# Kernel optimization log

Measured on AMD Instinct MI355X. Metric: run time of the kernel, lower is better.

The kernel has to match this reference:

```python
import math
import jax, jax.numpy as jnp
import numpy as np

B, S, M, D, H, FF = 2, 2048, 64, 1024, 16, 4096
HD = D // H


def setup_inputs() -> dict:
    key = jax.random.key(0)
    ks = jax.random.split(key, 16)
    w = lambda k, shape: jax.random.normal(k, shape, dtype=jnp.float32) * 0.02
    # RoPE angles: theta_i = pos / 10000^(2i/head_dim)
    inv_freq = 1.0 / (10000.0 ** (jnp.arange(0, HD, 2, dtype=jnp.float32) / HD))
    ang = jnp.arange(S, dtype=jnp.float32)[:, None] * inv_freq[None, :]  # (S, HD//2)
    return {
        "tgt": jax.random.normal(ks[0], (B, S, D), dtype=jnp.float32),
        "memory": jax.random.normal(ks[1], (B, M, D), dtype=jnp.float32),
        "rope_cos": jnp.cos(ang),
        "rope_sin": jnp.sin(ang),
        "W_qkv": w(ks[2], (D, 3 * D)), "b_qkv": jnp.zeros((3 * D,), jnp.float32),
        "W_o": w(ks[3], (D, D)), "b_o": jnp.zeros((D,), jnp.float32),
        "Wq_c": w(ks[4], (D, D)), "bq_c": jnp.zeros((D,), jnp.float32),
        "Wk_c": w(ks[5], (D, D)), "bk_c": jnp.zeros((D,), jnp.float32),
        "Wv_c": w(ks[6], (D, D)), "bv_c": jnp.zeros((D,), jnp.float32),
        "W_co": w(ks[7], (D, D)), "b_co": jnp.zeros((D,), jnp.float32),
        "W1": w(ks[8], (D, FF)), "b1": jnp.zeros((FF,), jnp.float32),
        "W2": w(ks[9], (FF, D)), "b2": jnp.zeros((D,), jnp.float32),
        "g1": jnp.ones((D,), jnp.float32), "be1": jnp.zeros((D,), jnp.float32),
        "g2": jnp.ones((D,), jnp.float32), "be2": jnp.zeros((D,), jnp.float32),
        "g3": jnp.ones((D,), jnp.float32), "be3": jnp.zeros((D,), jnp.float32),
    }


def _layer_norm(x, g, b, eps=1e-5):
    mu = jnp.mean(x, axis=-1, keepdims=True)
    var = jnp.mean(jnp.square(x - mu), axis=-1, keepdims=True)
    return (x - mu) * jax.lax.rsqrt(var + eps) * g + b


def _apply_rope(x, cos, sin):
    # x: (B, H, S, HD); cos/sin: (S, HD//2). Pairs (even, odd) rotated as complex.
    xe, xo = x[..., 0::2], x[..., 1::2]
    c = cos[None, None]
    s = sin[None, None]
    re = xe * c - xo * s
    im = xe * s + xo * c
    return jnp.stack([re, im], axis=-1).reshape(x.shape)


def reference(tgt, memory, rope_cos, rope_sin, W_qkv, b_qkv, W_o, b_o,
              Wq_c, bq_c, Wk_c, bk_c, Wv_c, bv_c, W_co, b_co,
              W1, b1, W2, b2, g1, be1, g2, be2, g3, be3):
    b, s, d = tgt.shape
    scale = 1.0 / math.sqrt(HD)

    # --- RoPE self-attention (causal) ---
    x = _layer_norm(tgt, g1, be1)
    qkv = (x @ W_qkv + b_qkv).reshape(b, s, 3, H, HD)
    qkv = jnp.transpose(qkv, (2, 0, 3, 1, 4))  # (3, b, H, s, HD)
    q, k, v = qkv[0], qkv[1], qkv[2]
    q = _apply_rope(q, rope_cos[:s], rope_sin[:s])
    k = _apply_rope(k, rope_cos[:s], rope_sin[:s])
    attn = jnp.einsum('bhqd,bhkd->bhqk', q, k) * scale
    causal = jnp.tril(jnp.ones((s, s), dtype=bool))
    attn = jnp.where(causal[None, None], attn, -1e9)
    attn = jax.nn.softmax(attn, axis=-1)
    sa = jnp.einsum('bhqk,bhkd->bhqd', attn, v)
    sa = jnp.transpose(sa, (0, 2, 1, 3)).reshape(b, s, d)
    tgt = tgt + (sa @ W_o + b_o)

    # --- cross-attention to memory (no positional encoding) ---
    x = _layer_norm(tgt, g2, be2)
    m = memory.shape[1]
    qc = (x @ Wq_c + bq_c).reshape(b, s, H, HD).transpose(0, 2, 1, 3)
    kc = (memory @ Wk_c + bk_c).reshape(b, m, H, HD).transpose(0, 2, 1, 3)
    vc = (memory @ Wv_c + bv_c).reshape(b, m, H, HD).transpose(0, 2, 1, 3)
    ca = jax.nn.softmax(jnp.einsum('bhqd,bhkd->bhqk', qc, kc) * scale, axis=-1)
    co = jnp.einsum('bhqk,bhkd->bhqd', ca, vc)
    co = jnp.transpose(co, (0, 2, 1, 3)).reshape(b, s, d)
    tgt = tgt + (co @ W_co + b_co)

    # --- FFN (exact GELU, dropout disabled = eval) ---
    x = _layer_norm(tgt, g3, be3)
    ffn = jax.nn.gelu(x @ W1 + b1, approximate=False) @ W2 + b2
    return tgt + ffn
```

## Files before the change

### kernel.cpp

```cpp
#include <hip/hip_runtime.h>

typedef unsigned short u16;
typedef short bf16x8 __attribute__((ext_vector_type(8)));
typedef float f32x4 __attribute__((ext_vector_type(4)));

#define HN 16
#define SD 64
#define SEQ 2048
#define DM 1024
#define QSC 0.18033688f

__device__ __forceinline__ float bf2f(u16 h) {
  return __uint_as_float(((unsigned int)h) << 16);
}
__device__ __forceinline__ u16 f2bf(float f) {
  unsigned int x = __float_as_uint(f);
  x += 0x7fffu + ((x >> 16) & 1u);
  return (u16)(x >> 16);
}
__device__ __forceinline__ float geluf(float x) {
  return 0.5f * x * (1.0f + erff(x * 0.70710678118654752f));
}
__device__ __forceinline__ void load_lds16(const u16* g, u16* l) {
  __builtin_amdgcn_global_load_lds(
      (const __attribute__((address_space(1))) void*)g,
      (__attribute__((address_space(3))) void*)l, 16, 0, 0);
}

__device__ __forceinline__ void trans_tile(const float* __restrict__ in,
                                           u16* __restrict__ out, int K, int N,
                                           int tx, int ty, int tid,
                                           u16 (*T)[72]) {
  const int n0 = tx * 64, k0 = ty * 64;
#pragma unroll
  for (int it = 0; it < 2; ++it) {
    const int t = it * 256 + tid, r = t >> 3, c = (t & 7) * 8;
    const float* src = &in[(size_t)(k0 + r) * N + n0 + c];
    float4 d0 = *(const float4*)src;
    float4 d1 = *(const float4*)(src + 4);
    T[r][c + 0] = f2bf(d0.x);
    T[r][c + 1] = f2bf(d0.y);
    T[r][c + 2] = f2bf(d0.z);
    T[r][c + 3] = f2bf(d0.w);
    T[r][c + 4] = f2bf(d1.x);
    T[r][c + 5] = f2bf(d1.y);
    T[r][c + 6] = f2bf(d1.z);
    T[r][c + 7] = f2bf(d1.w);
  }
  __syncthreads();
#pragma unroll
  for (int it = 0; it < 2; ++it) {
    const int t = it * 256 + tid, r = t >> 3, c = (t & 7) * 8;
    uint4 d;
    u16* p = (u16*)&d;
#pragma unroll
    for (int j = 0; j < 8; ++j) p[j] = T[c + j][r];
    *(uint4*)&out[(size_t)(n0 + r) * K + k0 + c] = d;
  }
}

__global__ __launch_bounds__(256) void prep1(
    const float* __restrict__ Wqkv, const float* __restrict__ Wo,
    const float* __restrict__ Wqc, const float* __restrict__ Wkc,
    const float* __restrict__ Wvc, const float* __restrict__ Wco,
    u16* __restrict__ Tqkv, u16* __restrict__ To, u16* __restrict__ Tqc,
    u16* __restrict__ Tkc, u16* __restrict__ Tvc, u16* __restrict__ Tco,
    const float* __restrict__ mem, u16* __restrict__ memb) {
  __shared__ u16 T[64][72];
  const int t = blockIdx.x, tid = threadIdx.x;
  if (t < 768) {
    trans_tile(Wqkv, Tqkv, 1024, 3072, t % 48, t / 48, tid, T);
    return;
  }
  if (t < 2048) {
    const int u = t - 768, m = u >> 8, sub = u & 255;
    const float* in;
    u16* out;
    if (m == 0) { in = Wo; out = To; }
    else if (m == 1) { in = Wqc; out = Tqc; }
    else if (m == 2) { in = Wkc; out = Tkc; }
    else if (m == 3) { in = Wvc; out = Tvc; }
    else { in = Wco; out = Tco; }
    trans_tile(in, out, 1024, 1024, sub & 15, sub >> 4, tid, T);
    return;
  }
  const int i = ((t - 2048) * 256 + tid) * 4;
  float4 d = *(const float4*)&mem[i];
  uint2 o;
  u16* po = (u16*)&o;
  po[0] = f2bf(d.x);
  po[1] = f2bf(d.y);
  po[2] = f2bf(d.z);
  po[3] = f2bf(d.w);
  *(uint2*)&memb[i] = o;
}

__global__ __launch_bounds__(256) void prep2(const float* __restrict__ W1,
                                             const float* __restrict__ W2,
                                             u16* __restrict__ T1,
                                             u16* __restrict__ T2) {
  __shared__ u16 T[64][72];
  const int t = blockIdx.x, tid = threadIdx.x;
  if (t < 1024) {
    trans_tile(W1, T1, 1024, 4096, t & 63, t >> 6, tid, T);
  } else {
    const int u = t - 1024;
    trans_tile(W2, T2, 4096, 1024, u & 15, u >> 4, tid, T);
  }
}

__global__ __launch_bounds__(256) void ln_kernel(
    const float* __restrict__ x, const float* __restrict__ g,
    const float* __restrict__ be, u16* __restrict__ y) {
  const int row = blockIdx.x, tid = threadIdx.x;
  const float* xr = x + (size_t)row * DM;
  float4 d = *(const float4*)&xr[tid * 4];
  float v[4] = {d.x, d.y, d.z, d.w};
  float s1 = 0.f, s2 = 0.f;
#pragma unroll
  for (int j = 0; j < 4; ++j) {
    s1 += v[j];
    s2 += v[j] * v[j];
  }
#pragma unroll
  for (int dd = 1; dd < 64; dd <<= 1) {
    s1 += __shfl_xor(s1, dd, 64);
    s2 += __shfl_xor(s2, dd, 64);
  }
  __shared__ float p1[4], p2[4];
  const int lane = tid & 63, wv = tid >> 6;
  if (lane == 0) {
    p1[wv] = s1;
    p2[wv] = s2;
  }
  __syncthreads();
  s1 = p1[0] + p1[1] + p1[2] + p1[3];
  s2 = p2[0] + p2[1] + p2[2] + p2[3];
  const float mu = s1 * (1.f / DM);
  const float rs = rsqrtf(fmaxf(s2 * (1.f / DM) - mu * mu, 0.f) + 1e-5f);
  float4 gg = *(const float4*)&g[tid * 4];
  float4 bb = *(const float4*)&be[tid * 4];
  const float gv[4] = {gg.x, gg.y, gg.z, gg.w};
  const float bv[4] = {bb.x, bb.y, bb.z, bb.w};
  uint2 o;
  u16* po = (u16*)&o;
#pragma unroll
  for (int j = 0; j < 4; ++j) po[j] = f2bf((v[j] - mu) * rs * gv[j] + bv[j]);
  *(uint2*)&y[(size_t)row * DM + tid * 4] = o;
}

template <int EPI, int TM>
__global__ __launch_bounds__(256) void gemm_bt(
    const u16* __restrict__ A, const u16* __restrict__ Bt,
    const float* __restrict__ bias, const float* __restrict__ resid,
    void* __restrict__ C0, u16* __restrict__ C1, u16* __restrict__ C2, int M,
    int N, int K, int rpbl, float sc, const float* __restrict__ rcos,
    const float* __restrict__ rsin) {
  constexpr int MI = TM / 32;
  __shared__ __align__(16) u16 As[TM][64];
  __shared__ __align__(16) u16 Bs[128][64];
  const int tid = threadIdx.x;
  const int lane = tid & 63, wv = tid >> 6;
  const int l16 = lane & 15, quad = lane >> 4;

  if (EPI == 6 && blockIdx.z) {
    Bt = (const u16*)C1;
    bias = resid;
  }

  int bx = blockIdx.x, by = blockIdx.y;
  const int gx = gridDim.x, gy = gridDim.y;
  if ((gy & 7) == 0) {
    const int f = by * gx + bx;
    const int c = f & 7, j = f >> 3;
    const int jm = j / gx;
    by = c * (gy >> 3) + jm;
    bx = j - jm * gx;
  }
  const int m0 = by * TM, n0 = bx * 128;
  const int wm = (wv >> 1) * (TM / 2), wn = (wv & 1) * 64;

  const int srow = lane >> 3;
  const int sblk = (lane & 7) ^ srow;
  const u16* ag[MI];
  const u16* bg[4];
  u16* la[MI];
  u16* lb[4];
#pragma unroll
  for (int i = 0; i < MI; ++i) {
    const int r0 = i * 32 + wv * 8;
    ag[i] = A + (size_t)(m0 + r0 + srow) * K + sblk * 8;
    la[i] = &As[r0][0] + lane * 8;
  }
#pragma unroll
  for (int i = 0; i < 4; ++i) {
    const int r0 = i * 32 + wv * 8;
    bg[i] = Bt + (size_t)(n0 + r0 + srow) * K + sblk * 8;
    lb[i] = &Bs[r0][0] + lane * 8;
  }

  f32x4 acc[MI][4] = {};

  for (int k0 = 0; k0 < K; k0 += 64) {
    __syncthreads();
#pragma unroll
    for (int i = 0; i < MI; ++i) load_lds16(ag[i] + k0, la[i]);
#pragma unroll
    for (int i = 0; i < 4; ++i) load_lds16(bg[i] + k0, lb[i]);
    __syncthreads();
#pragma unroll
    for (int kk = 0; kk < 2; ++kk) {
      bf16x8 af[MI], bfr[4];
#pragma unroll
      for (int mi = 0; mi < MI; ++mi) {
        const int row = wm + mi * 16 + l16;
        const int blk = (kk * 4 + quad) ^ (row & 7);
        af[mi] = *(const bf16x8*)&As[row][blk * 8];
      }
#pragma unroll
      for (int ni = 0; ni < 4; ++ni) {
        const int row = wn + ni * 16 + l16;
        const int blk = (kk * 4 + quad) ^ (row & 7);
        bfr[ni] = *(const bf16x8*)&Bs[row][blk * 8];
      }
#pragma unroll
      for (int mi = 0; mi < MI; ++mi)
#pragma unroll
        for (int ni = 0; ni < 4; ++ni)
          acc[mi][ni] = __builtin_amdgcn_mfma_f32_16x16x32_bf16(
              af[mi], bfr[ni], acc[mi][ni], 0, 0, 0);
    }
  }

  const int SL = 1 << rpbl;
#pragma unroll
  for (int mi = 0; mi < MI; ++mi) {
#pragma unroll
    for (int ni = 0; ni < 4; ++ni) {
#pragma unroll
      for (int r = 0; r < 4; ++r) {
        const int row = m0 + wm + mi * 16 + quad * 4 + r;
        const int col = n0 + wn + ni * 16 + l16;
        float vv = acc[mi][ni][r] + bias[col];
        if (EPI == 1) {
          vv += resid[(size_t)row * N + col];
          ((float*)C0)[(size_t)row * N + col] = vv;
        } else if (EPI == 2) {
          ((u16*)C0)[(size_t)row * N + col] = f2bf(geluf(vv));
        } else if (EPI == 3) {
          const float partner = __shfl_xor(vv, 1);
          const int which = col >> 10;
          const int nn = col & 1023;
          const int h = nn >> 6, hd = nn & 63;
          const int b = row >> rpbl;
          const int s = row & (SL - 1);
          if (which == 2) {
            C2[(((size_t)b * HN + h) * SD + hd) * SL + s] = f2bf(vv);
          } else {
            const int p = hd >> 1;
            const float cv = rcos[s * 32 + p];
            const float sv2 = rsin[s * 32 + p];
            float o = (hd & 1) ? (partner * sv2 + vv * cv)
                               : (vv * cv - partner * sv2);
            if (which == 0) o *= QSC;
            u16* dst = (which == 0) ? (u16*)C0 : C1;
            dst[(((size_t)b * HN + h) * SL + s) * SD + hd] = f2bf(o);
          }
        } else if (EPI == 4) {
          vv *= sc;
          const int h = col >> 6, hd = col & 63;
          const int b = row >> rpbl;
          const int s = row & (SL - 1);
          ((u16*)C0)[(((size_t)b * HN + h) * SL + s) * SD + hd] = f2bf(vv);
        } else if (EPI == 5) {
          const int h = col >> 6, hd = col & 63;
          const int b = row >> rpbl;
          const int s = row & (SL - 1);
          ((u16*)C0)[(((size_t)b * HN + h) * SD + hd) * SL + s] = f2bf(vv);
        } else if (EPI == 6) {
          const int h = col >> 6, hd = col & 63;
          const int b = row >> rpbl;
          const int s = row & (SL - 1);
          if (blockIdx.z == 0)
            ((u16*)C0)[(((size_t)b * HN + h) * SL + s) * SD + hd] = f2bf(vv);
          else
            C2[(((size_t)b * HN + h) * SD + hd) * SL + s] = f2bf(vv);
        } else {
          ((u16*)C0)[(size_t)row * N + col] = f2bf(vv);
        }
      }
    }
  }
}

template <int CAUSAL>
__global__ __launch_bounds__(512, 4) void attn_kernel(
    const u16* __restrict__ q, const u16* __restrict__ k,
    const u16* __restrict__ vt, u16* __restrict__ out, int kv_len) {
  __shared__ u16 Qs[64][72];
  __shared__ u16 Ks[128][72];
  __shared__ u16 VTs[64][136];
  __shared__ u16 Ps[128][68];
  const int tid = threadIdx.x;
  const int lane = tid & 63, wv = tid >> 6;
  const int t2 = wv >> 2, w4 = wv & 3;
  const int l16 = lane & 15, quad = lane >> 4;
  const int qt = blockIdx.x, bh = blockIdx.y;
  const u16* qb = q + ((size_t)bh * SEQ + qt * 64) * SD;
  const u16* kb = k + (size_t)bh * kv_len * SD;
  const u16* vtb = vt + (size_t)bh * SD * kv_len;

  {
    const int r = tid >> 3, c = (tid & 7) * 8;
    *(uint4*)&Qs[r][c] = *(const uint4*)&qb[(size_t)r * SD + c];
  }

  f32x4 o_acc[4] = {};
  float l_i[4] = {};

  const int nround =
      CAUSAL ? ((qt >> 1) + 1) : ((kv_len + 127) >> 7);
  const int kr = tid >> 2, kc4 = (tid & 3) * 16;
  const int vr = tid >> 3, vc16 = (tid & 7) * 16;

  for (int rd = 0; rd < nround; ++rd) {
    const int c0 = rd << 7;
    uint4 ka0 = {0, 0, 0, 0}, ka1 = {0, 0, 0, 0};
    uint4 va0 = {0, 0, 0, 0}, va1 = {0, 0, 0, 0};
    if (c0 + kr < kv_len) {
      ka0 = *(const uint4*)&kb[(size_t)(c0 + kr) * SD + kc4];
      ka1 = *(const uint4*)&kb[(size_t)(c0 + kr) * SD + kc4 + 8];
    }
    if (c0 + vc16 < kv_len) {
      va0 = *(const uint4*)&vtb[(size_t)vr * kv_len + c0 + vc16];
      va1 = *(const uint4*)&vtb[(size_t)vr * kv_len + c0 + vc16 + 8];
    }
    __syncthreads();
    *(uint4*)&Ks[kr][kc4] = ka0;
    *(uint4*)&Ks[kr][kc4 + 8] = ka1;
    *(uint4*)&VTs[vr][vc16] = va0;
    *(uint4*)&VTs[vr][vc16 + 8] = va1;
    __syncthreads();

    const int st = (rd << 1) + t2;
    const bool part = CAUSAL ? (st <= qt) : (st * 64 < kv_len);
    if (part) {
      f32x4 s_acc[4] = {};
#pragma unroll
      for (int kk = 0; kk < 64; kk += 32) {
        const bf16x8 aq = *(const bf16x8*)&Qs[w4 * 16 + l16][kk + quad * 8];
#pragma unroll
        for (int ni = 0; ni < 4; ++ni) {
          const bf16x8 bk =
              *(const bf16x8*)&Ks[t2 * 64 + ni * 16 + l16][kk + quad * 8];
          s_acc[ni] = __builtin_amdgcn_mfma_f32_16x16x32_bf16(aq, bk, s_acc[ni],
                                                              0, 0, 0);
        }
      }
      float rsum[4] = {0.f, 0.f, 0.f, 0.f};
      const bool dg = CAUSAL && (st == qt);
#pragma unroll
      for (int ni = 0; ni < 4; ++ni)
#pragma unroll
        for (int r = 0; r < 4; ++r) {
          float sv = s_acc[ni][r];
          if (dg && (ni * 16 + l16 > w4 * 16 + quad * 4 + r)) sv = -1e9f;
          const float pe = __builtin_amdgcn_exp2f(sv);
          rsum[r] += pe;
          Ps[wv * 16 + quad * 4 + r][ni * 16 + l16] =
              (u16)(__float_as_uint(pe) >> 16);
        }
#pragma unroll
      for (int r = 0; r < 4; ++r) {
#pragma unroll
        for (int dd = 1; dd < 16; dd <<= 1)
          rsum[r] += __shfl_xor(rsum[r], dd, 64);
        l_i[r] += rsum[r];
      }
#pragma unroll
      for (int kk = 0; kk < 64; kk += 32) {
        const bf16x8 ap = *(const bf16x8*)&Ps[wv * 16 + l16][kk + quad * 8];
#pragma unroll
        for (int ni = 0; ni < 4; ++ni) {
          const bf16x8 bv =
              *(const bf16x8*)&VTs[ni * 16 + l16][t2 * 64 + kk + quad * 8];
          o_acc[ni] = __builtin_amdgcn_mfma_f32_16x16x32_bf16(ap, bv, o_acc[ni],
                                                              0, 0, 0);
        }
      }
    }
  }

  __syncthreads();
  float* Omb = (float*)&Ks[0][0];
  float* lbuf = (float*)&VTs[0][0];
  if (t2 == 1) {
#pragma unroll
    for (int r = 0; r < 4; ++r) {
      const int row = w4 * 16 + quad * 4 + r;
      if (l16 == 0) lbuf[row] = l_i[r];
#pragma unroll
      for (int ni = 0; ni < 4; ++ni)
        Omb[row * 68 + ni * 16 + l16] = o_acc[ni][r];
    }
  }
  __syncthreads();
  if (t2 == 0) {
    const int b = bh >> 4, h = bh & 15;
#pragma unroll
    for (int r = 0; r < 4; ++r) {
      const int row = w4 * 16 + quad * 4 + r;
      const float inv = 1.f / (l_i[r] + lbuf[row]);
      const int s = qt * 64 + row;
#pragma unroll
      for (int ni = 0; ni < 4; ++ni) {
        const float val = o_acc[ni][r] + Omb[row * 68 + ni * 16 + l16];
        out[((size_t)b * SEQ + s) * DM + h * SD + ni * 16 + l16] =
            f2bf(val * inv);
      }
    }
  }
}

extern "C" void kernel_launch(void* const* d_in, const int* in_sizes, int n_in,
                              void* d_out, int out_size, void* d_ws,
                              size_t ws_size, hipStream_t stream) {
  (void)in_sizes;
  (void)n_in;
  (void)out_size;
  (void)ws_size;
  const float* tgt = (const float*)d_in[0];
  const float* mem = (const float*)d_in[1];
  const float* rc = (const float*)d_in[2];
  const float* rsn = (const float*)d_in[3];
  const float* W_qkv = (const float*)d_in[4];
  const float* b_qkv = (const float*)d_in[5];
  const float* W_o = (const float*)d_in[6];
  const float* b_o = (const float*)d_in[7];
  const float* Wq_c = (const float*)d_in[8];
  const float* bq_c = (const float*)d_in[9];
  const float* Wk_c = (const float*)d_in[10];
  const float* bk_c = (const float*)d_in[11];
  const float* Wv_c = (const float*)d_in[12];
  const float* bv_c = (const float*)d_in[13];
  const float* W_co = (const float*)d_in[14];
  const float* b_co = (const float*)d_in[15];
  const float* W1 = (const float*)d_in[16];
  const float* b1 = (const float*)d_in[17];
  const float* W2 = (const float*)d_in[18];
  const float* b2 = (const float*)d_in[19];
  const float* g1 = (const float*)d_in[20];
  const float* be1 = (const float*)d_in[21];
  const float* g2 = (const float*)d_in[22];
  const float* be2 = (const float*)d_in[23];
  const float* g3 = (const float*)d_in[24];
  const float* be3 = (const float*)d_in[25];

  const size_t M1 = 1048576;
  u16* w = (u16*)d_ws;
  u16* WTqkv = w;
  u16* WTo = w + 3 * M1;
  u16* WTqc = w + 4 * M1;
  u16* WTkc = w + 5 * M1;
  u16* WTvc = w + 6 * M1;
  u16* WTco = w + 7 * M1;
  u16* WT1 = w;
  u16* WT2 = w + 4 * M1;
  u16* xb = w + 8 * M1;
  u16* qb = w + 12 * M1;
  u16* kb = w + 16 * M1;
  u16* vbT = w + 20 * M1;
  u16* at = w + 24 * M1;
  u16* kc = w + 28 * M1;
  u16* vcT = kc + 131072;
  u16* memb = vcT + 131072;
  u16* ffh = qb;
  float* res = (float*)d_out;

  dim3 blk(256), blk512(512);
  prep1<<<2176, blk, 0, stream>>>(W_qkv, W_o, Wq_c, Wk_c, Wv_c, W_co, WTqkv,
                                  WTo, WTqc, WTkc, WTvc, WTco, mem, memb);

  ln_kernel<<<4096, blk, 0, stream>>>(tgt, g1, be1, xb);
  gemm_bt<3, 128><<<dim3(24, 32), blk, 0, stream>>>(
      xb, WTqkv, b_qkv, nullptr, qb, kb, vbT, 4096, 3072, 1024, 11, 1.f, rc,
      rsn);
  attn_kernel<1><<<dim3(32, 32), blk512, 0, stream>>>(qb, kb, vbT, at, 2048);
  gemm_bt<1, 64><<<dim3(8, 64), blk, 0, stream>>>(at, WTo, b_o, tgt, res,
                                                  nullptr, nullptr, 4096, 1024,
                                                  1024, 0, 1.f, nullptr,
                                                  nullptr);
  ln_kernel<<<4096, blk, 0, stream>>>(res, g2, be2, xb);
  gemm_bt<4, 64><<<dim3(8, 64), blk, 0, stream>>>(
      xb, WTqc, bq_c, nullptr, qb, nullptr, nullptr, 4096, 1024, 1024, 11, QSC,
      nullptr, nullptr);
  gemm_bt<6, 64><<<dim3(8, 2, 2), blk, 0, stream>>>(
      memb, WTkc, bk_c, bv_c, kc, WTvc, vcT, 128, 1024, 1024, 6, 1.f, nullptr,
      nullptr);
  attn_kernel<0><<<dim3(32, 32), blk512, 0, stream>>>(qb, kc, vcT, at, 64);
  gemm_bt<1, 64><<<dim3(8, 64), blk, 0, stream>>>(at, WTco, b_co, res, res,
                                                  nullptr, nullptr, 4096, 1024,
                                                  1024, 0, 1.f, nullptr,
                                                  nullptr);
  prep2<<<2048, blk, 0, stream>>>(W1, W2, WT1, WT2);
  ln_kernel<<<4096, blk, 0, stream>>>(res, g3, be3, xb);
  gemm_bt<2, 128><<<dim3(32, 32), blk, 0, stream>>>(
      xb, WT1, b1, nullptr, ffh, nullptr, nullptr, 4096, 4096, 1024, 0, 1.f,
      nullptr, nullptr);
  gemm_bt<1, 64><<<dim3(8, 64), blk, 0, stream>>>(ffh, WT2, b2, res, res,
                                                  nullptr, nullptr, 4096, 1024,
                                                  4096, 0, 1.f, nullptr,
                                                  nullptr);
}
```

Baseline: 548.1 us.

## Pair complementary causal query tiles per attention block and drop split-KV merge

Each attention block now handles two query tiles (qt and 31-qt for causal, or qt and qt+16 for cross-attention). The two wave halves share each 64-key K/V tile loaded into LDS, instead of splitting the keys across halves and merging partial results through LDS at the end. This balances causal work across blocks, halves the grid, and removes the final reduction and its barriers. In exchange, the per-iteration K/V tile is smaller and sync points per key increase, and for causal the qtA half sits idle on tiles past its diagonal.

```diff
diff --git a/kernel.cpp b/kernel.cpp
--- a/kernel.cpp
+++ b/kernel.cpp
@@ -297,68 +297,56 @@
 __global__ __launch_bounds__(512, 4) void attn_kernel(
     const u16* __restrict__ q, const u16* __restrict__ k,
     const u16* __restrict__ vt, u16* __restrict__ out, int kv_len) {
-  __shared__ u16 Qs[64][72];
-  __shared__ u16 Ks[128][72];
-  __shared__ u16 VTs[64][136];
+  __shared__ u16 Qs[128][72], Ks[64][72], VTs[64][72];
   __shared__ u16 Ps[128][68];
   const int tid = threadIdx.x;
   const int lane = tid & 63, wv = tid >> 6;
   const int t2 = wv >> 2, w4 = wv & 3;
   const int l16 = lane & 15, quad = lane >> 4;
-  const int qt = blockIdx.x, bh = blockIdx.y;
-  const u16* qb = q + ((size_t)bh * SEQ + qt * 64) * SD;
+  const int bx = blockIdx.x, bh = blockIdx.y;
+  const int qtA = bx;
+  const int qtB = CAUSAL ? (31 - bx) : (bx + 16);
+  const int qt = t2 ? qtB : qtA;
+  const u16* qb = q + (size_t)bh * SEQ * SD;
   const u16* kb = k + (size_t)bh * kv_len * SD;
   const u16* vtb = vt + (size_t)bh * SD * kv_len;
 
-  {
-    const int r = tid >> 3, c = (tid & 7) * 8;
-    *(uint4*)&Qs[r][c] = *(const uint4*)&qb[(size_t)r * SD + c];
+#pragma unroll
+  for (int it = 0; it < 2; ++it) {
+    const int t = it * 512 + tid, r = t >> 3, c = (t & 7) * 8;
+    const int qrow = (r < 64) ? (qtA * 64 + r) : (qtB * 64 + (r - 64));
+    *(uint4*)&Qs[r][c] = *(const uint4*)&qb[(size_t)qrow * SD + c];
   }
 
   f32x4 o_acc[4] = {};
   float l_i[4] = {};
 
-  const int nround =
-      CAUSAL ? ((qt >> 1) + 1) : ((kv_len + 127) >> 7);
-  const int kr = tid >> 2, kc4 = (tid & 3) * 16;
-  const int vr = tid >> 3, vc16 = (tid & 7) * 16;
-
-  for (int rd = 0; rd < nround; ++rd) {
-    const int c0 = rd << 7;
-    uint4 ka0 = {0, 0, 0, 0}, ka1 = {0, 0, 0, 0};
-    uint4 va0 = {0, 0, 0, 0}, va1 = {0, 0, 0, 0};
-    if (c0 + kr < kv_len) {
-      ka0 = *(const uint4*)&kb[(size_t)(c0 + kr) * SD + kc4];
-      ka1 = *(const uint4*)&kb[(size_t)(c0 + kr) * SD + kc4 + 8];
-    }
-    if (c0 + vc16 < kv_len) {
-      va0 = *(const uint4*)&vtb[(size_t)vr * kv_len + c0 + vc16];
-      va1 = *(const uint4*)&vtb[(size_t)vr * kv_len + c0 + vc16 + 8];
-    }
+  const int ktiles = CAUSAL ? (qtB + 1) : ((kv_len + 63) >> 6);
+  const int sr = tid >> 3, sc8 = (tid & 7) * 8;
+
+  for (int kt = 0; kt < ktiles; ++kt) {
+    const uint4 kd = *(const uint4*)&kb[((size_t)kt * 64 + sr) * SD + sc8];
+    const uint4 vd = *(const uint4*)&vtb[(size_t)sr * kv_len + kt * 64 + sc8];
     __syncthreads();
-    *(uint4*)&Ks[kr][kc4] = ka0;
-    *(uint4*)&Ks[kr][kc4 + 8] = ka1;
-    *(uint4*)&VTs[vr][vc16] = va0;
-    *(uint4*)&VTs[vr][vc16 + 8] = va1;
+    *(uint4*)&Ks[sr][sc8] = kd;
+    *(uint4*)&VTs[sr][sc8] = vd;
     __syncthreads();
 
-    const int st = (rd << 1) + t2;
-    const bool part = CAUSAL ? (st <= qt) : (st * 64 < kv_len);
-    if (part) {
+    if (kt <= qt) {
+      const int roff = t2 * 64 + w4 * 16;
       f32x4 s_acc[4] = {};
 #pragma unroll
       for (int kk = 0; kk < 64; kk += 32) {
-        const bf16x8 aq = *(const bf16x8*)&Qs[w4 * 16 + l16][kk + quad * 8];
+        const bf16x8 aq = *(const bf16x8*)&Qs[roff + l16][kk + quad * 8];
 #pragma unroll
         for (int ni = 0; ni < 4; ++ni) {
-          const bf16x8 bk =
-              *(const bf16x8*)&Ks[t2 * 64 + ni * 16 + l16][kk + quad * 8];
+          const bf16x8 bk = *(const bf16x8*)&Ks[ni * 16 + l16][kk + quad * 8];
           s_acc[ni] = __builtin_amdgcn_mfma_f32_16x16x32_bf16(aq, bk, s_acc[ni],
                                                               0, 0, 0);
         }
       }
       float rsum[4] = {0.f, 0.f, 0.f, 0.f};
-      const bool dg = CAUSAL && (st == qt);
+      const bool dg = CAUSAL && (kt == qt);
 #pragma unroll
       for (int ni = 0; ni < 4; ++ni)
 #pragma unroll
@@ -382,8 +370,7 @@
         const bf16x8 ap = *(const bf16x8*)&Ps[wv * 16 + l16][kk + quad * 8];
 #pragma unroll
         for (int ni = 0; ni < 4; ++ni) {
-          const bf16x8 bv =
-              *(const bf16x8*)&VTs[ni * 16 + l16][t2 * 64 + kk + quad * 8];
+          const bf16x8 bv = *(const bf16x8*)&VTs[ni * 16 + l16][kk + quad * 8];
           o_acc[ni] = __builtin_amdgcn_mfma_f32_16x16x32_bf16(ap, bv, o_acc[ni],
                                                               0, 0, 0);
         }
@@ -391,34 +378,15 @@
     }
   }
 
-  __syncthreads();
-  float* Omb = (float*)&Ks[0][0];
-  float* lbuf = (float*)&VTs[0][0];
-  if (t2 == 1) {
-#pragma unroll
-    for (int r = 0; r < 4; ++r) {
-      const int row = w4 * 16 + quad * 4 + r;
-      if (l16 == 0) lbuf[row] = l_i[r];
-#pragma unroll
-      for (int ni = 0; ni < 4; ++ni)
-        Omb[row * 68 + ni * 16 + l16] = o_acc[ni][r];
-    }
-  }
-  __syncthreads();
-  if (t2 == 0) {
-    const int b = bh >> 4, h = bh & 15;
-#pragma unroll
-    for (int r = 0; r < 4; ++r) {
-      const int row = w4 * 16 + quad * 4 + r;
-      const float inv = 1.f / (l_i[r] + lbuf[row]);
-      const int s = qt * 64 + row;
-#pragma unroll
-      for (int ni = 0; ni < 4; ++ni) {
-        const float val = o_acc[ni][r] + Omb[row * 68 + ni * 16 + l16];
-        out[((size_t)b * SEQ + s) * DM + h * SD + ni * 16 + l16] =
-            f2bf(val * inv);
-      }
-    }
+  const int b = bh >> 4, h = bh & 15;
+#pragma unroll
+  for (int r = 0; r < 4; ++r) {
+    const float inv = 1.f / l_i[r];
+    const int s = qt * 64 + w4 * 16 + quad * 4 + r;
+#pragma unroll
+    for (int ni = 0; ni < 4; ++ni)
+      out[((size_t)b * SEQ + s) * DM + h * SD + ni * 16 + l16] =
+          f2bf(o_acc[ni][r] * inv);
   }
 }
 
@@ -485,7 +453,7 @@
   gemm_bt<3, 128><<<dim3(24, 32), blk, 0, stream>>>(
       xb, WTqkv, b_qkv, nullptr, qb, kb, vbT, 4096, 3072, 1024, 11, 1.f, rc,
       rsn);
-  attn_kernel<1><<<dim3(32, 32), blk512, 0, stream>>>(qb, kb, vbT, at, 2048);
+  attn_kernel<1><<<dim3(16, 32), blk512, 0, stream>>>(qb, kb, vbT, at, 2048);
   gemm_bt<1, 64><<<dim3(8, 64), blk, 0, stream>>>(at, WTo, b_o, tgt, res,
                                                   nullptr, nullptr, 4096, 1024,
                                                   1024, 0, 1.f, nullptr,
@@ -497,7 +465,7 @@
   gemm_bt<6, 64><<<dim3(8, 2, 2), blk, 0, stream>>>(
       memb, WTkc, bk_c, bv_c, kc, WTvc, vcT, 128, 1024, 1024, 6, 1.f, nullptr,
       nullptr);
-  attn_kernel<0><<<dim3(32, 32), blk512, 0, stream>>>(qb, kc, vcT, at, 64);
+  attn_kernel<0><<<dim3(16, 32), blk512, 0, stream>>>(qb, kc, vcT, at, 64);
   gemm_bt<1, 64><<<dim3(8, 64), blk, 0, stream>>>(at, WTco, b_co, res, res,
                                                   nullptr, nullptr, 4096, 1024,
                                                   1024, 0, 1.f, nullptr,
```

Measured after the change: 510.0 us. 1.07x faster.
